# Performance work log

Hardware: AMD Instinct MI355X
Metric: run time of the kernel (lower is better)

Reference implementation:

```python
import jax, jax.numpy as jnp
import numpy as np

N_NODES = 20000
N_EDGES = 160000
N_GRAPHS = 16
NEG_INF = -1e30


def gcn_conv(x, edge_index, edge_weight, W, b):
    # PyG GCNConv with improved=True: add self-loops with weight 2.0,
    # symmetric degree normalization, linear transform, scatter-add aggregation.
    N = x.shape[0]
    row, col = edge_index[0], edge_index[1]
    loop = jnp.arange(N)
    row = jnp.concatenate([row, loop])
    col = jnp.concatenate([col, loop])
    ew = jnp.concatenate([edge_weight, jnp.full((N,), 2.0, edge_weight.dtype)])
    deg = jax.ops.segment_sum(ew, col, num_segments=N)
    dinv = jnp.where(deg > 0, deg ** -0.5, 0.0)  # deg_inv_sqrt, inf -> 0
    norm = dinv[row] * ew * dinv[col]            # [E+N]
    xl = x @ W                                   # [N, out]
    out = jax.ops.segment_sum(xl[row] * norm[:, None], col, num_segments=N)
    return out + b


def segment_softmax_masked(logits, mask, batch, num_segments):
    # softmax over masked entries, grouped by graph id (torch_geometric softmax
    # after masked_select); unmasked-out positions return 0.
    neg = jnp.asarray(NEG_INF, logits.dtype)
    ml = jnp.where(mask, logits, neg)
    mx = jax.ops.segment_max(ml, batch, num_segments=num_segments)
    ex = jnp.where(mask, jnp.exp(logits - mx[batch]), 0.0)
    s = jax.ops.segment_sum(ex, batch, num_segments=num_segments)
    return ex / jnp.maximum(s[batch], 1e-16)


def setup_inputs() -> dict:
    key = jax.random.key(0)
    ks = jax.random.split(key, 12)
    x = jax.random.normal(ks[0], (N_NODES, 5), dtype=jnp.float32)
    edge_index = jax.random.randint(ks[1], (2, N_EDGES), 0, N_NODES)
    edge_weight = jax.random.uniform(ks[2], (N_EDGES,), dtype=jnp.float32)
    mask = jax.random.randint(ks[3], (N_NODES,), 0, 2).astype(bool)
    batch = jnp.sort(jax.random.randint(ks[4], (N_NODES,), 0, N_GRAPHS))
    # parameters (Glorot-ish scaling)
    W1 = jax.random.normal(ks[5], (5, 1000), dtype=jnp.float32) / np.sqrt(5)
    b1 = jnp.zeros((1000,), jnp.float32)
    W2 = jax.random.normal(ks[6], (1000, 1000), dtype=jnp.float32) / np.sqrt(1000)
    b2 = jnp.zeros((1000,), jnp.float32)
    Wf = jax.random.normal(ks[7], (1000, 1), dtype=jnp.float32) / np.sqrt(1000)
    bf = jnp.zeros((1,), jnp.float32)
    return {"x": x, "edge_weight": edge_weight, "W1": W1, "b1": b1,
            "W2": W2, "b2": b2, "Wf": Wf, "bf": bf,
            "edge_index": edge_index, "mask": mask, "batch": batch}


def reference(x, edge_weight, W1, b1, W2, b2, Wf, bf, edge_index, mask, batch):
    h = jax.nn.relu(gcn_conv(x, edge_index, edge_weight, W1, b1))
    h = jax.nn.relu(gcn_conv(h, edge_index, edge_weight, W2, b2))
    # dropout treated as identity (eval mode) for a deterministic reference
    logits = (h @ Wf + bf)[:, 0]  # [N]
    return segment_softmax_masked(logits, mask, batch, N_GRAPHS)
```

## Files before the change

kernel.cpp:

```cpp
#include <hip/hip_runtime.h>

#define NN 20000
#define NE 160000
#define NG 16
#define KP 1024
#define MT2 160
#define MPAD2 (MT2*128)
#define NBLK 79

typedef __attribute__((ext_vector_type(8))) short bf16x8;
typedef __attribute__((ext_vector_type(4))) float f32x4;

#define GAS __attribute__((address_space(1)))
#define LAS __attribute__((address_space(3)))

__device__ __forceinline__ unsigned short f2bf(float f) {
    unsigned int u = __float_as_uint(f);
    u += 0x7FFFu + ((u >> 16) & 1u);
    return (unsigned short)(u >> 16);
}

__device__ __forceinline__ float bf2f(unsigned short u) {
    return __uint_as_float(((unsigned)u) << 16);
}

__device__ __forceinline__ void gld_lds16(const char* g, char* l) {
    __builtin_amdgcn_global_load_lds((GAS void*)g, (LAS void*)l, 16, 0, 0);
}

__global__ void deg_cnt_kernel(const int* __restrict__ ei, const float* __restrict__ ew,
                               float* deg, int* cnt, const void* __restrict__ mask,
                               int* flags) {
    const int e = blockIdx.x * blockDim.x + threadIdx.x;
    if (e < 5000) {
        const unsigned v = ((const unsigned*)mask)[e];
        if (v > 1u) atomicOr(&flags[0], 1);
        if (v != 0u && v != 0x3F800000u) atomicOr(&flags[1], 1);
    }
    if (e >= NE) return;
    const int c = ei[NE + e];
    atomicAdd(&deg[c], ew[e]);
    atomicAdd(&cnt[c], 1);
}

__global__ __launch_bounds__(256) void partial_kernel(const int* __restrict__ cnt,
        const float* __restrict__ deg, const void* __restrict__ mask,
        const int* __restrict__ flags, int* __restrict__ mtmp,
        float* __restrict__ dinv, int* __restrict__ bcnt, int* __restrict__ bmsk) {
    const int b = blockIdx.x, t = threadIdx.x;
    const int i = b * 256 + t;
    const int f0 = flags[0], f1 = flags[1];
    int c = 0, mv = 0;
    if (i < NN) {
        c = cnt[i];
        dinv[i] = 1.0f / sqrtf(2.0f + deg[i]);
        if (f0 == 0)      mv = ((const int*)mask)[i] != 0;
        else if (f1 == 0) mv = ((const unsigned*)mask)[i] != 0u;
        else              mv = ((const unsigned char*)mask)[i] != 0;
        mtmp[i] = mv;
    }
    __shared__ int sc[256], sm[256];
    sc[t] = c; sm[t] = mv;
    __syncthreads();
    for (int off = 128; off; off >>= 1) {
        if (t < off) { sc[t] += sc[t + off]; sm[t] += sm[t + off]; }
        __syncthreads();
    }
    if (t == 0) { bcnt[b] = sc[0]; bmsk[b] = sm[0]; }
}

__global__ __launch_bounds__(128) void scanp_kernel(int* __restrict__ bcnt,
        int* __restrict__ bmsk, int* __restrict__ nm) {
    const int t = threadIdx.x;
    __shared__ int sc[128], sm[128];
    const int c = (t < NBLK) ? bcnt[t] : 0;
    const int m = (t < NBLK) ? bmsk[t] : 0;
    sc[t] = c; sm[t] = m;
    __syncthreads();
    for (int off = 1; off < 128; off <<= 1) {
        const int uc = (t >= off) ? sc[t - off] : 0;
        const int um = (t >= off) ? sm[t - off] : 0;
        __syncthreads();
        sc[t] += uc; sm[t] += um;
        __syncthreads();
    }
    if (t < NBLK) { bcnt[t] = sc[t] - c; bmsk[t] = sm[t] - m; }
    if (t == NBLK - 1) nm[0] = sm[t];
}

__global__ __launch_bounds__(256) void apply_kernel(const int* __restrict__ cnt,
        const int* __restrict__ mtmp, const int* __restrict__ bcnt,
        const int* __restrict__ bmsk, const int* __restrict__ batch,
        int* __restrict__ offs, int* __restrict__ perm, int* __restrict__ bc) {
    const int b = blockIdx.x, t = threadIdx.x;
    const int i = b * 256 + t;
    const int c  = (i < NN) ? cnt[i]  : 0;
    const int mv = (i < NN) ? mtmp[i] : 0;
    __shared__ int sc[256], sm[256];
    sc[t] = c; sm[t] = mv;
    __syncthreads();
    for (int off = 1; off < 256; off <<= 1) {
        const int uc = (t >= off) ? sc[t - off] : 0;
        const int um = (t >= off) ? sm[t - off] : 0;
        __syncthreads();
        sc[t] += uc; sm[t] += um;
        __syncthreads();
    }
    if (i < NN) {
        offs[i] = bcnt[b] + sc[t] - c;
        if (mv) {
            const int pos = bmsk[b] + sm[t] - 1;
            perm[pos] = i;
            bc[pos] = batch[i];
        }
    }
}

__global__ void scatter_kernel(const int* __restrict__ ei, const float* __restrict__ ew,
                               const float* __restrict__ dinv, const int* __restrict__ offs,
                               int* cursor, int* __restrict__ ssrc, float* __restrict__ snorm) {
    const int e = blockIdx.x * blockDim.x + threadIdx.x;
    if (e >= NE) return;
    const int r = ei[e], c = ei[NE + e];
    const int pos = atomicAdd(&cursor[c], 1);
    const int idx = offs[c] + pos;
    ssrc[idx] = r;
    snorm[idx] = dinv[r] * ew[e] * dinv[c];
}

__global__ __launch_bounds__(256) void ax_kernel(const float* __restrict__ x,
        const int* __restrict__ ssrc, const float* __restrict__ snorm,
        const int* __restrict__ offs, const int* __restrict__ cnt,
        float* __restrict__ Ax) {
    const int i = blockIdx.x * blockDim.x + threadIdx.x;
    if (i >= NN) return;
    float a0=0,a1=0,a2=0,a3=0,a4=0;
    const int s0 = offs[i], n = cnt[i];
    for (int e = s0; e < s0 + n; ++e) {
        const int r = ssrc[e];
        const float w = snorm[e];
        const float* xr = x + r * 5;
        a0 += w*xr[0]; a1 += w*xr[1]; a2 += w*xr[2]; a3 += w*xr[3]; a4 += w*xr[4];
    }
    float* o = Ax + i * 5;
    o[0]=a0; o[1]=a1; o[2]=a2; o[3]=a3; o[4]=a4;
}

__global__ __launch_bounds__(256) void prep_kernel(const float* __restrict__ Ax,
        const float* __restrict__ x, const float* __restrict__ dinv,
        const float* __restrict__ W1, const float* __restrict__ b1,
        unsigned short* __restrict__ h1,
        const float* __restrict__ W2, unsigned short* __restrict__ W2t) {
    const int bid = blockIdx.x;
    const int t = threadIdx.x;
    if (bid < 1250) {
        __shared__ float w1s[5000];
        __shared__ float axs[80];
        for (int idx = t; idx < 1250; idx += 256)
            ((float4*)w1s)[idx] = ((const float4*)W1)[idx];
        const int nb = bid * 16;
        if (t < 80) {
            const int node = nb + t / 5;
            const float dv = dinv[node];
            axs[t] = Ax[nb * 5 + t] + 2.0f * dv * dv * x[nb * 5 + t];
        }
        __syncthreads();
        if (t < 250) {
            const int c0 = t * 4;
            float w[5][4];
#pragma unroll
            for (int f = 0; f < 5; ++f) {
                const float4 wv = ((const float4*)w1s)[f * 250 + t];
                w[f][0] = wv.x; w[f][1] = wv.y; w[f][2] = wv.z; w[f][3] = wv.w;
            }
            const float4 bb = *(const float4*)(b1 + c0);
            for (int n = 0; n < 16; ++n) {
                float r0 = bb.x, r1 = bb.y, r2 = bb.z, r3 = bb.w;
#pragma unroll
                for (int f = 0; f < 5; ++f) {
                    const float av = axs[n * 5 + f];
                    r0 += av * w[f][0]; r1 += av * w[f][1];
                    r2 += av * w[f][2]; r3 += av * w[f][3];
                }
                ushort4 pk;
                pk.x = f2bf(fmaxf(r0, 0.f)); pk.y = f2bf(fmaxf(r1, 0.f));
                pk.z = f2bf(fmaxf(r2, 0.f)); pk.w = f2bf(fmaxf(r3, 0.f));
                *(ushort4*)(h1 + (size_t)(nb + n) * KP + c0) = pk;
            }
        } else {
            const int c0 = 1000 + (t - 250) * 4;
            ushort4 zz = {0, 0, 0, 0};
            for (int n = 0; n < 16; ++n)
                *(ushort4*)(h1 + (size_t)(nb + n) * KP + c0) = zz;
        }
    } else {
        __shared__ float tile[32][33];
        const int bw = bid - 1250;
        const int n0 = (bw & 31) * 32;
        const int k0 = (bw >> 5) * 32;
        const int tx = t & 31, ty = t >> 5;
#pragma unroll
        for (int j = 0; j < 4; ++j) {
            const int k = k0 + ty + j * 8;
            const int n = n0 + tx;
            tile[ty + j * 8][tx] = (k < 1000 && n < 1000) ? W2[k * 1000 + n] : 0.0f;
        }
        __syncthreads();
#pragma unroll
        for (int j = 0; j < 4; ++j) {
            const int n = n0 + ty + j * 8;
            const int k = k0 + tx;
            W2t[(size_t)n * KP + k] = f2bf(tile[tx][ty + j * 8]);
        }
    }
}

__global__ __launch_bounds__(256) void agg1k_kernel(const unsigned short* __restrict__ h1,
        const int* __restrict__ ssrc, const float* __restrict__ snorm,
        const int* __restrict__ offs, const int* __restrict__ cnt,
        const float* __restrict__ dinv, const int* __restrict__ perm,
        const int* __restrict__ nm, unsigned short* __restrict__ G) {
    const int j0 = blockIdx.x;
    const int t = threadIdx.x;
    __shared__ int s_nm;
    if (t == 0) s_nm = nm[0];
    __syncthreads();
    const int nmv = s_nm;
    const int npad = (nmv + 127) & ~127;
    if (j0 >= npad) return;
    const int sub = t >> 7;
    const int tc = t & 127;
    unsigned short* grow = G + (size_t)j0 * KP + tc * 8;
    if (j0 >= nmv) {
        if (sub == 0) {
            bf16x8 z = {0,0,0,0,0,0,0,0};
            *(bf16x8*)grow = z;
        }
        return;
    }
    const int i = perm[j0];
    __shared__ int   se[64];
    __shared__ float sw[64];
    float acc[8] = {0,0,0,0,0,0,0,0};
    float acc2[8] = {0,0,0,0,0,0,0,0};
    const int s0 = offs[i], n = cnt[i];
    for (int base = 0; base < n; base += 64) {
        const int m = (n - base < 64) ? (n - base) : 64;
        __syncthreads();
        if (t < m) { se[t] = ssrc[s0 + base + t]; sw[t] = snorm[s0 + base + t]; }
        __syncthreads();
        int e = sub;
        for (; e + 2 < m; e += 4) {
            const int r0 = se[e];     const float w0 = sw[e];
            const int r1 = se[e + 2]; const float w1 = sw[e + 2];
            const bf16x8 v0 = *(const bf16x8*)(h1 + (size_t)r0 * KP + tc * 8);
            const bf16x8 v1 = *(const bf16x8*)(h1 + (size_t)r1 * KP + tc * 8);
#pragma unroll
            for (int jj = 0; jj < 8; ++jj) acc[jj]  += w0 * bf2f((unsigned short)v0[jj]);
#pragma unroll
            for (int jj = 0; jj < 8; ++jj) acc2[jj] += w1 * bf2f((unsigned short)v1[jj]);
        }
        for (; e < m; e += 2) {
            const int r = se[e];
            const float w = sw[e];
            const bf16x8 hv = *(const bf16x8*)(h1 + (size_t)r * KP + tc * 8);
#pragma unroll
            for (int jj = 0; jj < 8; ++jj) acc[jj] += w * bf2f((unsigned short)hv[jj]);
        }
    }
    if (sub == 0) {
        const float wl = 2.0f * dinv[i] * dinv[i];
        const bf16x8 hv = *(const bf16x8*)(h1 + (size_t)i * KP + tc * 8);
#pragma unroll
        for (int jj = 0; jj < 8; ++jj) acc[jj] += wl * bf2f((unsigned short)hv[jj]);
    }
#pragma unroll
    for (int jj = 0; jj < 8; ++jj) acc[jj] += acc2[jj];
    __shared__ float red[128][8];
    if (sub == 1) {
#pragma unroll
        for (int jj = 0; jj < 8; ++jj) red[tc][jj] = acc[jj];
    }
    __syncthreads();
    if (sub == 0) {
        bf16x8 o;
#pragma unroll
        for (int jj = 0; jj < 8; ++jj) o[jj] = (short)f2bf(acc[jj] + red[tc][jj]);
        *(bf16x8*)grow = o;
    }
}

__global__ __launch_bounds__(256) void gemm_kernel(const unsigned short* __restrict__ A,
                                                   const unsigned short* __restrict__ B,
                                                   const float* __restrict__ b2,
                                                   const float* __restrict__ Wf,
                                                   const int* __restrict__ nm,
                                                   float* __restrict__ logitsC) {
    __shared__ unsigned short As[4096];
    __shared__ unsigned short Bs[4096];
    const int tid = threadIdx.x;
    __shared__ int s_nm;
    if (tid == 0) s_nm = nm[0];
    __syncthreads();
    const int nmv = s_nm;
    const int mstrips = (nmv + 127) >> 7;
    const int bid = blockIdx.x;
    const int tm = (bid >> 6) * 8 + (bid & 7);
    const int tn = (bid >> 3) & 7;
    if (tm >= mstrips) return;
    const int lane = tid & 63;
    const int wv = tid >> 6;
    const int wr = wv >> 1, wc = wv & 1;

    const int chunk = ((tid & 3) ^ ((tid >> 3) & 3)) * 16;
    const int rsub = tid >> 2;
    const char* Ag = (const char*)(A + (size_t)(tm * 128 + rsub) * KP) + chunk;
    const char* Bg = (const char*)(B + (size_t)(tn * 128 + rsub) * KP) + chunk;
    char* AsW = (char*)As + wv * 1024;
    char* BsW = (char*)Bs + wv * 1024;

    f32x4 acc[4][4];
#pragma unroll
    for (int i = 0; i < 4; ++i)
#pragma unroll
        for (int j = 0; j < 4; ++j) acc[i][j] = (f32x4){0.f, 0.f, 0.f, 0.f};

    const int m = lane & 15;
    const int quad = lane >> 4;
    const int sw = quad ^ ((m >> 1) & 3);
    const int aoff = (wr * 64 + m) * 64 + sw * 16;
    const int boff = (wc * 64 + m) * 64 + sw * 16;

    for (int kk = 0; kk < KP; kk += 32) {
        __syncthreads();
        const int kb = kk * 2;
        gld_lds16(Ag + kb,             AsW);
        gld_lds16(Ag + kb + 64 * 2048, AsW + 4096);
        gld_lds16(Bg + kb,             BsW);
        gld_lds16(Bg + kb + 64 * 2048, BsW + 4096);
        __syncthreads();
        bf16x8 af[4], bfv[4];
#pragma unroll
        for (int mt = 0; mt < 4; ++mt)
            af[mt] = *(const bf16x8*)((const char*)As + aoff + mt * 1024);
#pragma unroll
        for (int nt = 0; nt < 4; ++nt)
            bfv[nt] = *(const bf16x8*)((const char*)Bs + boff + nt * 1024);
#pragma unroll
        for (int mt = 0; mt < 4; ++mt)
#pragma unroll
            for (int nt = 0; nt < 4; ++nt)
                acc[mt][nt] = __builtin_amdgcn_mfma_f32_16x16x32_bf16(af[mt], bfv[nt], acc[mt][nt], 0, 0, 0);
    }

    const int col0 = tn * 128 + wc * 64 + m;
    const int row00 = tm * 128 + wr * 64 + quad * 4;
#pragma unroll
    for (int mt = 0; mt < 4; ++mt) {
        float ps0 = 0.f, ps1 = 0.f, ps2 = 0.f, ps3 = 0.f;
#pragma unroll
        for (int nt = 0; nt < 4; ++nt) {
            const int c = col0 + nt * 16;
            const float bb = (c < 1000) ? b2[c] : 0.0f;
            const float wf = (c < 1000) ? Wf[c] : 0.0f;
            ps0 += fmaxf(acc[mt][nt][0] + bb, 0.f) * wf;
            ps1 += fmaxf(acc[mt][nt][1] + bb, 0.f) * wf;
            ps2 += fmaxf(acc[mt][nt][2] + bb, 0.f) * wf;
            ps3 += fmaxf(acc[mt][nt][3] + bb, 0.f) * wf;
        }
#pragma unroll
        for (int msk = 1; msk < 16; msk <<= 1) {
            ps0 += __shfl_xor(ps0, msk);
            ps1 += __shfl_xor(ps1, msk);
            ps2 += __shfl_xor(ps2, msk);
            ps3 += __shfl_xor(ps3, msk);
        }
        if (m == 0) {
            const int row = row00 + mt * 16;
            if (row + 0 < nmv) atomicAdd(&logitsC[row + 0], ps0);
            if (row + 1 < nmv) atomicAdd(&logitsC[row + 1], ps1);
            if (row + 2 < nmv) atomicAdd(&logitsC[row + 2], ps2);
            if (row + 3 < nmv) atomicAdd(&logitsC[row + 3], ps3);
        }
    }
}

__global__ __launch_bounds__(256) void softmax_kernel(const float* __restrict__ logitsC,
        const int* __restrict__ perm, const int* __restrict__ bc,
        const int* __restrict__ nm, float* __restrict__ out) {
    const int g = blockIdx.x;
    const int t = threadIdx.x;
    __shared__ int s_lo, s_hi;
    __shared__ float red[4];
    __shared__ float sval;
    if (t == 0) {
        const int nmv = nm[0];
        int lo = 0, hi = nmv;
        while (lo < hi) { const int mid = (lo + hi) >> 1; if (bc[mid] < g) lo = mid + 1; else hi = mid; }
        s_lo = lo;
        int lo2 = lo, hi2 = nmv;
        while (lo2 < hi2) { const int mid = (lo2 + hi2) >> 1; if (bc[mid] < g + 1) lo2 = mid + 1; else hi2 = mid; }
        s_hi = lo2;
    }
    __syncthreads();
    const int lo = s_lo, hi = s_hi;
    float mx = -1e30f;
    for (int i = lo + t; i < hi; i += 256) mx = fmaxf(mx, logitsC[i]);
    for (int off = 32; off; off >>= 1) mx = fmaxf(mx, __shfl_down(mx, off));
    if ((t & 63) == 0) red[t >> 6] = mx;
    __syncthreads();
    if (t == 0) sval = fmaxf(fmaxf(red[0], red[1]), fmaxf(red[2], red[3]));
    __syncthreads();
    mx = sval;
    __syncthreads();
    float sm = 0.f;
    for (int i = lo + t; i < hi; i += 256) sm += expf(logitsC[i] - mx);
    for (int off = 32; off; off >>= 1) sm += __shfl_down(sm, off);
    if ((t & 63) == 0) red[t >> 6] = sm;
    __syncthreads();
    if (t == 0) sval = red[0] + red[1] + red[2] + red[3];
    __syncthreads();
    const float inv = 1.0f / fmaxf(sval, 1e-16f);
    for (int i = lo + t; i < hi; i += 256)
        out[perm[i]] = expf(logitsC[i] - mx) * inv;
}

extern "C" void kernel_launch(void* const* d_in, const int* in_sizes, int n_in,
                              void* d_out, int out_size, void* d_ws, size_t ws_size,
                              hipStream_t stream) {
    (void)in_sizes; (void)n_in; (void)ws_size;
    const float* x   = (const float*)d_in[0];
    const float* ew  = (const float*)d_in[1];
    const float* W1  = (const float*)d_in[2];
    const float* b1  = (const float*)d_in[3];
    const float* W2  = (const float*)d_in[4];
    const float* b2  = (const float*)d_in[5];
    const float* Wf  = (const float*)d_in[6];
    const int*   ei  = (const int*)d_in[8];
    const void*  mask  = d_in[9];
    const int*   batch = (const int*)d_in[10];
    float* out = (float*)d_out;

    char* p = (char*)d_ws;
    auto carve = [&](size_t bytes) { char* q = p; p += (bytes + 255) & ~(size_t)255; return q; };
    char* zbase = p;
    float* deg     = (float*)carve(NN * 4);
    int*   cnt     = (int*)carve(NN * 4);
    int*   cursor  = (int*)carve(NN * 4);
    float* logitsC = (float*)carve(MPAD2 * 4);
    int*   flags   = (int*)carve(256);
    size_t zspan = (size_t)(p - zbase);
    int*   offs   = (int*)carve(NN * 4);
    float* dinv   = (float*)carve(NN * 4);
    int*   mtmp   = (int*)carve(NN * 4);
    int*   perm   = (int*)carve(NN * 4);
    int*   bc     = (int*)carve(NN * 4);
    int*   bcnt   = (int*)carve(NBLK * 4);
    int*   bmsk   = (int*)carve(NBLK * 4);
    int*   nmp    = (int*)carve(256);
    int*   ssrc   = (int*)carve(NE * 4);
    float* snorm  = (float*)carve(NE * 4);
    float* Ax     = (float*)carve(NN * 5 * 4);
    unsigned short* W2t = (unsigned short*)carve((size_t)KP * KP * 2);
    unsigned short* h1  = (unsigned short*)carve((size_t)NN * KP * 2);
    unsigned short* G   = (unsigned short*)carve((size_t)MPAD2 * KP * 2);

    hipMemsetAsync(zbase, 0, zspan, stream);
    hipMemsetAsync(out, 0, (size_t)out_size * 4, stream);
    hipLaunchKernelGGL(deg_cnt_kernel,  dim3(625),   dim3(256),  0, stream, ei, ew, deg, cnt, mask, flags);
    hipLaunchKernelGGL(partial_kernel,  dim3(NBLK),  dim3(256),  0, stream, cnt, deg, mask, flags, mtmp, dinv, bcnt, bmsk);
    hipLaunchKernelGGL(scanp_kernel,    dim3(1),     dim3(128),  0, stream, bcnt, bmsk, nmp);
    hipLaunchKernelGGL(apply_kernel,    dim3(NBLK),  dim3(256),  0, stream, cnt, mtmp, bcnt, bmsk, batch, offs, perm, bc);
    hipLaunchKernelGGL(scatter_kernel,  dim3(625),   dim3(256),  0, stream, ei, ew, dinv, offs, cursor, ssrc, snorm);
    hipLaunchKernelGGL(ax_kernel,       dim3(79),    dim3(256),  0, stream, x, ssrc, snorm, offs, cnt, Ax);
    hipLaunchKernelGGL(prep_kernel,     dim3(2274),  dim3(256),  0, stream, Ax, x, dinv, W1, b1, h1, W2, W2t);
    hipLaunchKernelGGL(agg1k_kernel,    dim3(MPAD2), dim3(256),  0, stream, h1, ssrc, snorm, offs, cnt, dinv, perm, nmp, G);
    hipLaunchKernelGGL(gemm_kernel,     dim3(MT2*8), dim3(256),  0, stream, G, W2t, b2, Wf, nmp, logitsC);
    hipLaunchKernelGGL(softmax_kernel,  dim3(NG),    dim3(256),  0, stream, logitsC, perm, bc, nmp, out);
}
```

Before: 205.5 us.

## Recompute layer-1 activations on the fly during layer-2 aggregation instead of materializing h1

```diff
diff --git a/kernel.cpp b/kernel.cpp
--- a/kernel.cpp
+++ b/kernel.cpp
@@ -18,10 +18,6 @@
     unsigned int u = __float_as_uint(f);
     u += 0x7FFFu + ((u >> 16) & 1u);
     return (unsigned short)(u >> 16);
-}
-
-__device__ __forceinline__ float bf2f(unsigned short u) {
-    return __uint_as_float(((unsigned)u) << 16);
 }
 
 __device__ __forceinline__ void gld_lds16(const char* g, char* l) {
@@ -128,10 +124,10 @@
     snorm[idx] = dinv[r] * ew[e] * dinv[c];
 }
 
-__global__ __launch_bounds__(256) void ax_kernel(const float* __restrict__ x,
+__global__ __launch_bounds__(256) void axf_kernel(const float* __restrict__ x,
         const int* __restrict__ ssrc, const float* __restrict__ snorm,
         const int* __restrict__ offs, const int* __restrict__ cnt,
-        float* __restrict__ Ax) {
+        const float* __restrict__ dinv, float* __restrict__ Axf) {
     const int i = blockIdx.x * blockDim.x + threadIdx.x;
     if (i >= NN) return;
     float a0=0,a1=0,a2=0,a3=0,a4=0;
@@ -142,151 +138,115 @@
         const float* xr = x + r * 5;
         a0 += w*xr[0]; a1 += w*xr[1]; a2 += w*xr[2]; a3 += w*xr[3]; a4 += w*xr[4];
     }
-    float* o = Ax + i * 5;
+    const float wl = 2.0f * dinv[i] * dinv[i];
+    const float* xi = x + i * 5;
+    a0 += wl*xi[0]; a1 += wl*xi[1]; a2 += wl*xi[2]; a3 += wl*xi[3]; a4 += wl*xi[4];
+    float* o = Axf + i * 5;
     o[0]=a0; o[1]=a1; o[2]=a2; o[3]=a3; o[4]=a4;
 }
 
-__global__ __launch_bounds__(256) void prep_kernel(const float* __restrict__ Ax,
-        const float* __restrict__ x, const float* __restrict__ dinv,
+__global__ __launch_bounds__(256) void w2t_kernel(const float* __restrict__ W2,
+                                                  unsigned short* __restrict__ W2t) {
+    __shared__ float tile[32][33];
+    const int bw = blockIdx.x;
+    const int n0 = (bw & 31) * 32;
+    const int k0 = (bw >> 5) * 32;
+    const int t = threadIdx.x;
+    const int tx = t & 31, ty = t >> 5;
+#pragma unroll
+    for (int j = 0; j < 4; ++j) {
+        const int k = k0 + ty + j * 8;
+        const int n = n0 + tx;
+        tile[ty + j * 8][tx] = (k < 1000 && n < 1000) ? W2[k * 1000 + n] : 0.0f;
+    }
+    __syncthreads();
+#pragma unroll
+    for (int j = 0; j < 4; ++j) {
+        const int n = n0 + ty + j * 8;
+        const int k = k0 + tx;
+        W2t[(size_t)n * KP + k] = f2bf(tile[tx][ty + j * 8]);
+    }
+}
+
+__global__ __launch_bounds__(256) void aggW1_kernel(const float* __restrict__ Axf,
         const float* __restrict__ W1, const float* __restrict__ b1,
-        unsigned short* __restrict__ h1,
-        const float* __restrict__ W2, unsigned short* __restrict__ W2t) {
-    const int bid = blockIdx.x;
-    const int t = threadIdx.x;
-    if (bid < 1250) {
-        __shared__ float w1s[5000];
-        __shared__ float axs[80];
-        for (int idx = t; idx < 1250; idx += 256)
-            ((float4*)w1s)[idx] = ((const float4*)W1)[idx];
-        const int nb = bid * 16;
-        if (t < 80) {
-            const int node = nb + t / 5;
-            const float dv = dinv[node];
-            axs[t] = Ax[nb * 5 + t] + 2.0f * dv * dv * x[nb * 5 + t];
-        }
-        __syncthreads();
-        if (t < 250) {
-            const int c0 = t * 4;
-            float w[5][4];
-#pragma unroll
-            for (int f = 0; f < 5; ++f) {
-                const float4 wv = ((const float4*)w1s)[f * 250 + t];
-                w[f][0] = wv.x; w[f][1] = wv.y; w[f][2] = wv.z; w[f][3] = wv.w;
-            }
-            const float4 bb = *(const float4*)(b1 + c0);
-            for (int n = 0; n < 16; ++n) {
-                float r0 = bb.x, r1 = bb.y, r2 = bb.z, r3 = bb.w;
-#pragma unroll
-                for (int f = 0; f < 5; ++f) {
-                    const float av = axs[n * 5 + f];
-                    r0 += av * w[f][0]; r1 += av * w[f][1];
-                    r2 += av * w[f][2]; r3 += av * w[f][3];
-                }
-                ushort4 pk;
-                pk.x = f2bf(fmaxf(r0, 0.f)); pk.y = f2bf(fmaxf(r1, 0.f));
-                pk.z = f2bf(fmaxf(r2, 0.f)); pk.w = f2bf(fmaxf(r3, 0.f));
-                *(ushort4*)(h1 + (size_t)(nb + n) * KP + c0) = pk;
-            }
-        } else {
-            const int c0 = 1000 + (t - 250) * 4;
-            ushort4 zz = {0, 0, 0, 0};
-            for (int n = 0; n < 16; ++n)
-                *(ushort4*)(h1 + (size_t)(nb + n) * KP + c0) = zz;
-        }
-    } else {
-        __shared__ float tile[32][33];
-        const int bw = bid - 1250;
-        const int n0 = (bw & 31) * 32;
-        const int k0 = (bw >> 5) * 32;
-        const int tx = t & 31, ty = t >> 5;
-#pragma unroll
-        for (int j = 0; j < 4; ++j) {
-            const int k = k0 + ty + j * 8;
-            const int n = n0 + tx;
-            tile[ty + j * 8][tx] = (k < 1000 && n < 1000) ? W2[k * 1000 + n] : 0.0f;
-        }
-        __syncthreads();
-#pragma unroll
-        for (int j = 0; j < 4; ++j) {
-            const int n = n0 + ty + j * 8;
-            const int k = k0 + tx;
-            W2t[(size_t)n * KP + k] = f2bf(tile[tx][ty + j * 8]);
-        }
-    }
-}
-
-__global__ __launch_bounds__(256) void agg1k_kernel(const unsigned short* __restrict__ h1,
         const int* __restrict__ ssrc, const float* __restrict__ snorm,
         const int* __restrict__ offs, const int* __restrict__ cnt,
         const float* __restrict__ dinv, const int* __restrict__ perm,
         const int* __restrict__ nm, unsigned short* __restrict__ G) {
-    const int j0 = blockIdx.x;
     const int t = threadIdx.x;
     __shared__ int s_nm;
     if (t == 0) s_nm = nm[0];
     __syncthreads();
     const int nmv = s_nm;
     const int npad = (nmv + 127) & ~127;
+    const int j0 = blockIdx.x * 8;
     if (j0 >= npad) return;
-    const int sub = t >> 7;
-    const int tc = t & 127;
-    unsigned short* grow = G + (size_t)j0 * KP + tc * 8;
-    if (j0 >= nmv) {
-        if (sub == 0) {
-            bf16x8 z = {0,0,0,0,0,0,0,0};
-            *(bf16x8*)grow = z;
-        }
-        return;
-    }
-    const int i = perm[j0];
+
+    const bool active = t < 250;
+    const int c0 = active ? t * 4 : 1000 + (t - 250) * 4;
+    float w[5][4];
+    float bb[4];
+    if (active) {
+#pragma unroll
+        for (int f = 0; f < 5; ++f) {
+            const float4 wv = *(const float4*)(W1 + f * 1000 + c0);
+            w[f][0] = wv.x; w[f][1] = wv.y; w[f][2] = wv.z; w[f][3] = wv.w;
+        }
+        const float4 b4 = *(const float4*)(b1 + c0);
+        bb[0] = b4.x; bb[1] = b4.y; bb[2] = b4.z; bb[3] = b4.w;
+    } else {
+#pragma unroll
+        for (int f = 0; f < 5; ++f) { w[f][0]=0; w[f][1]=0; w[f][2]=0; w[f][3]=0; }
+        bb[0]=0; bb[1]=0; bb[2]=0; bb[3]=0;
+    }
+
     __shared__ int   se[64];
     __shared__ float sw[64];
-    float acc[8] = {0,0,0,0,0,0,0,0};
-    float acc2[8] = {0,0,0,0,0,0,0,0};
-    const int s0 = offs[i], n = cnt[i];
-    for (int base = 0; base < n; base += 64) {
-        const int m = (n - base < 64) ? (n - base) : 64;
-        __syncthreads();
-        if (t < m) { se[t] = ssrc[s0 + base + t]; sw[t] = snorm[s0 + base + t]; }
-        __syncthreads();
-        int e = sub;
-        for (; e + 2 < m; e += 4) {
-            const int r0 = se[e];     const float w0 = sw[e];
-            const int r1 = se[e + 2]; const float w1 = sw[e + 2];
-            const bf16x8 v0 = *(const bf16x8*)(h1 + (size_t)r0 * KP + tc * 8);
-            const bf16x8 v1 = *(const bf16x8*)(h1 + (size_t)r1 * KP + tc * 8);
-#pragma unroll
-            for (int jj = 0; jj < 8; ++jj) acc[jj]  += w0 * bf2f((unsigned short)v0[jj]);
-#pragma unroll
-            for (int jj = 0; jj < 8; ++jj) acc2[jj] += w1 * bf2f((unsigned short)v1[jj]);
-        }
-        for (; e < m; e += 2) {
-            const int r = se[e];
-            const float w = sw[e];
-            const bf16x8 hv = *(const bf16x8*)(h1 + (size_t)r * KP + tc * 8);
-#pragma unroll
-            for (int jj = 0; jj < 8; ++jj) acc[jj] += w * bf2f((unsigned short)hv[jj]);
-        }
-    }
-    if (sub == 0) {
-        const float wl = 2.0f * dinv[i] * dinv[i];
-        const bf16x8 hv = *(const bf16x8*)(h1 + (size_t)i * KP + tc * 8);
-#pragma unroll
-        for (int jj = 0; jj < 8; ++jj) acc[jj] += wl * bf2f((unsigned short)hv[jj]);
-    }
-#pragma unroll
-    for (int jj = 0; jj < 8; ++jj) acc[jj] += acc2[jj];
-    __shared__ float red[128][8];
-    if (sub == 1) {
-#pragma unroll
-        for (int jj = 0; jj < 8; ++jj) red[tc][jj] = acc[jj];
-    }
-    __syncthreads();
-    if (sub == 0) {
-        bf16x8 o;
-#pragma unroll
-        for (int jj = 0; jj < 8; ++jj) o[jj] = (short)f2bf(acc[jj] + red[tc][jj]);
-        *(bf16x8*)grow = o;
+    for (int jj = 0; jj < 8; ++jj) {
+        const int j = j0 + jj;
+        if (j >= npad) break;
+        float acc0 = 0.f, acc1 = 0.f, acc2 = 0.f, acc3 = 0.f;
+        if (j < nmv) {
+            const int i = perm[j];
+            const int s0 = offs[i], n = cnt[i];
+            for (int base = 0; base < n; base += 64) {
+                const int m = (n - base < 64) ? (n - base) : 64;
+                __syncthreads();
+                if (t < m) { se[t] = ssrc[s0 + base + t]; sw[t] = snorm[s0 + base + t]; }
+                __syncthreads();
+                for (int e = 0; e < m; ++e) {
+                    const int r = se[e];
+                    const float we = sw[e];
+                    const float* axr = Axf + r * 5;
+                    float z0 = bb[0], z1 = bb[1], z2 = bb[2], z3 = bb[3];
+#pragma unroll
+                    for (int f = 0; f < 5; ++f) {
+                        const float a = axr[f];
+                        z0 += a * w[f][0]; z1 += a * w[f][1];
+                        z2 += a * w[f][2]; z3 += a * w[f][3];
+                    }
+                    acc0 += we * fmaxf(z0, 0.f); acc1 += we * fmaxf(z1, 0.f);
+                    acc2 += we * fmaxf(z2, 0.f); acc3 += we * fmaxf(z3, 0.f);
+                }
+            }
+            {
+                const float wl = 2.0f * dinv[i] * dinv[i];
+                const float* axi = Axf + i * 5;
+                float z0 = bb[0], z1 = bb[1], z2 = bb[2], z3 = bb[3];
+#pragma unroll
+                for (int f = 0; f < 5; ++f) {
+                    const float a = axi[f];
+                    z0 += a * w[f][0]; z1 += a * w[f][1];
+                    z2 += a * w[f][2]; z3 += a * w[f][3];
+                }
+                acc0 += wl * fmaxf(z0, 0.f); acc1 += wl * fmaxf(z1, 0.f);
+                acc2 += wl * fmaxf(z2, 0.f); acc3 += wl * fmaxf(z3, 0.f);
+            }
+        }
+        ushort4 pk;
+        pk.x = f2bf(acc0); pk.y = f2bf(acc1); pk.z = f2bf(acc2); pk.w = f2bf(acc3);
+        *(ushort4*)(G + (size_t)j * KP + c0) = pk;
     }
 }
 
@@ -361,12 +321,12 @@
 #pragma unroll
         for (int nt = 0; nt < 4; ++nt) {
             const int c = col0 + nt * 16;
-            const float bb = (c < 1000) ? b2[c] : 0.0f;
-            const float wf = (c < 1000) ? Wf[c] : 0.0f;
-            ps0 += fmaxf(acc[mt][nt][0] + bb, 0.f) * wf;
-            ps1 += fmaxf(acc[mt][nt][1] + bb, 0.f) * wf;
-            ps2 += fmaxf(acc[mt][nt][2] + bb, 0.f) * wf;
-            ps3 += fmaxf(acc[mt][nt][3] + bb, 0.f) * wf;
+            const float bbv = (c < 1000) ? b2[c] : 0.0f;
+            const float wfv = (c < 1000) ? Wf[c] : 0.0f;
+            ps0 += fmaxf(acc[mt][nt][0] + bbv, 0.f) * wfv;
+            ps1 += fmaxf(acc[mt][nt][1] + bbv, 0.f) * wfv;
+            ps2 += fmaxf(acc[mt][nt][2] + bbv, 0.f) * wfv;
+            ps3 += fmaxf(acc[mt][nt][3] + bbv, 0.f) * wfv;
         }
 #pragma unroll
         for (int msk = 1; msk < 16; msk <<= 1) {
@@ -460,21 +420,20 @@
     int*   nmp    = (int*)carve(256);
     int*   ssrc   = (int*)carve(NE * 4);
     float* snorm  = (float*)carve(NE * 4);
-    float* Ax     = (float*)carve(NN * 5 * 4);
+    float* Axf    = (float*)carve(NN * 5 * 4);
     unsigned short* W2t = (unsigned short*)carve((size_t)KP * KP * 2);
-    unsigned short* h1  = (unsigned short*)carve((size_t)NN * KP * 2);
     unsigned short* G   = (unsigned short*)carve((size_t)MPAD2 * KP * 2);
 
     hipMemsetAsync(zbase, 0, zspan, stream);
     hipMemsetAsync(out, 0, (size_t)out_size * 4, stream);
-    hipLaunchKernelGGL(deg_cnt_kernel,  dim3(625),   dim3(256),  0, stream, ei, ew, deg, cnt, mask, flags);
-    hipLaunchKernelGGL(partial_kernel,  dim3(NBLK),  dim3(256),  0, stream, cnt, deg, mask, flags, mtmp, dinv, bcnt, bmsk);
-    hipLaunchKernelGGL(scanp_kernel,    dim3(1),     dim3(128),  0, stream, bcnt, bmsk, nmp);
-    hipLaunchKernelGGL(apply_kernel,    dim3(NBLK),  dim3(256),  0, stream, cnt, mtmp, bcnt, bmsk, batch, offs, perm, bc);
-    hipLaunchKernelGGL(scatter_kernel,  dim3(625),   dim3(256),  0, stream, ei, ew, dinv, offs, cursor, ssrc, snorm);
-    hipLaunchKernelGGL(ax_kernel,       dim3(79),    dim3(256),  0, stream, x, ssrc, snorm, offs, cnt, Ax);
-    hipLaunchKernelGGL(prep_kernel,     dim3(2274),  dim3(256),  0, stream, Ax, x, dinv, W1, b1, h1, W2, W2t);
-    hipLaunchKernelGGL(agg1k_kernel,    dim3(MPAD2), dim3(256),  0, stream, h1, ssrc, snorm, offs, cnt, dinv, perm, nmp, G);
-    hipLaunchKernelGGL(gemm_kernel,     dim3(MT2*8), dim3(256),  0, stream, G, W2t, b2, Wf, nmp, logitsC);
-    hipLaunchKernelGGL(softmax_kernel,  dim3(NG),    dim3(256),  0, stream, logitsC, perm, bc, nmp, out);
-}
+    hipLaunchKernelGGL(deg_cnt_kernel,  dim3(625),      dim3(256),  0, stream, ei, ew, deg, cnt, mask, flags);
+    hipLaunchKernelGGL(partial_kernel,  dim3(NBLK),     dim3(256),  0, stream, cnt, deg, mask, flags, mtmp, dinv, bcnt, bmsk);
+    hipLaunchKernelGGL(scanp_kernel,    dim3(1),        dim3(128),  0, stream, bcnt, bmsk, nmp);
+    hipLaunchKernelGGL(apply_kernel,    dim3(NBLK),     dim3(256),  0, stream, cnt, mtmp, bcnt, bmsk, batch, offs, perm, bc);
+    hipLaunchKernelGGL(scatter_kernel,  dim3(625),      dim3(256),  0, stream, ei, ew, dinv, offs, cursor, ssrc, snorm);
+    hipLaunchKernelGGL(axf_kernel,      dim3(79),       dim3(256),  0, stream, x, ssrc, snorm, offs, cnt, dinv, Axf);
+    hipLaunchKernelGGL(w2t_kernel,      dim3(1024),     dim3(256),  0, stream, W2, W2t);
+    hipLaunchKernelGGL(aggW1_kernel,    dim3(MPAD2/8),  dim3(256),  0, stream, Axf, W1, b1, ssrc, snorm, offs, cnt, dinv, perm, nmp, G);
+    hipLaunchKernelGGL(gemm_kernel,     dim3(MT2*8),    dim3(256),  0, stream, G, W2t, b2, Wf, nmp, logitsC);
+    hipLaunchKernelGGL(softmax_kernel,  dim3(NG),       dim3(256),  0, stream, logitsC, perm, bc, nmp, out);
+}
```

Measured after the change: 213.8 us. 1.04x slower.
